# Kernel optimization log

Hardware: AMD Instinct MI355X
Metric: run time of the kernel (lower is better)

The kernel has to match this reference:

```python
import jax, jax.numpy as jnp
import numpy as np

P, F_IN, HG, C, T, E, HOUT = 4096, 64, 64, 64, 32, 65536, 12
LEAKY_SLOPE = 0.2
LN_EPS = 1e-5


def setup_inputs() -> dict:
    key = jax.random.key(0)
    ks = jax.random.split(key, 14)
    g = lambda k, shape, scale: (jax.random.normal(k, shape, jnp.float32) * scale)
    return {
        "X": jax.random.normal(ks[0], (1, P, F_IN, T), jnp.float32),
        "edge_index": jax.random.randint(ks[1], (T, 2, E), 0, P, jnp.int32),
        # GATv2 params (single head)
        "Wl": g(ks[2], (F_IN, HG), 0.1),
        "Wr": g(ks[3], (F_IN, HG), 0.1),
        "att": g(ks[4], (HG,), 0.1),
        "gat_b": g(ks[5], (HG,), 0.02),
        # 1x1 time conv (HG -> C) and 1x1 residual conv (F_IN -> C)
        "W_time": g(ks[6], (C, HG), 0.1),
        "b_time": g(ks[7], (C,), 0.02),
        "W_res": g(ks[8], (C, F_IN), 0.1),
        "b_res": g(ks[9], (C,), 0.02),
        # LayerNorm over channel dim C
        "ln_g": jnp.ones((C,), jnp.float32),
        "ln_b": jnp.zeros((C,), jnp.float32),
        # final conv: Conv2d(in=T, out=HOUT, kernel=(1, C)) -> weight (HOUT, T, C)
        "W_final": g(ks[10], (HOUT, T, C), 0.05),
        "b_final": g(ks[11], (HOUT,), 0.02),
    }


def reference(X, edge_index, Wl, Wr, att, gat_b, W_time, b_time, W_res, b_res,
              ln_g, ln_b, W_final, b_final):
    Pn = X.shape[1]

    def gat_t(x, edges):
        # x: (P, F_IN), edges: (2, E) with edges[0]=src j, edges[1]=dst i
        src, dst = edges[0], edges[1]
        hl = x @ Wl                      # (P, HG) messages
        hr = x @ Wr                      # (P, HG) query side
        e = jax.nn.leaky_relu(hl[src] + hr[dst], LEAKY_SLOPE) @ att  # (E,)
        emax = jax.ops.segment_max(e, dst, num_segments=Pn)
        ex = jnp.exp(e - emax[dst])
        den = jax.ops.segment_sum(ex, dst, num_segments=Pn)
        alpha = ex / den[dst]            # softmax over in-edges of each dst
        return jax.ops.segment_sum(alpha[:, None] * hl[src], dst,
                                   num_segments=Pn) + gat_b  # (P, HG)

    xs = jnp.moveaxis(X[0], -1, 0)                     # (T, P, F_IN)
    X_hat = jax.nn.relu(jax.vmap(gat_t)(xs, edge_index))  # (T, P, HG)

    th = jnp.einsum('tph,ch->tpc', X_hat, W_time) + b_time  # time conv 1x1
    rs = jnp.einsum('tpf,cf->tpc', xs, W_res) + b_res       # residual conv 1x1
    y = jax.nn.relu(th + rs)                                 # (T, P, C)

    mu = jnp.mean(y, axis=-1, keepdims=True)
    var = jnp.var(y, axis=-1, keepdims=True)
    yn = (y - mu) * jax.lax.rsqrt(var + LN_EPS) * ln_g + ln_b  # (T, P, C)

    # final conv: in-channels = T, kernel (1, C) -> contract over t and c
    out = jnp.einsum('tpc,otc->po', yn, W_final) + b_final     # (P, HOUT)
    return out[None]                                           # (1, P, HOUT)
```

## Files before the change

kernel.cpp:

```cpp
#include <hip/hip_runtime.h>
#include <math.h>

#define NP 4096
#define F_IN 64
#define HG 64
#define NC 64
#define NT 32
#define NE 65536
#define HOUT 12
#define LEAKY 0.2f
#define LN_EPS 1e-5f
#define CAPC 32

template <int CTRL>
__device__ __forceinline__ float dppadd(float v, float x) {
    int r = __builtin_amdgcn_update_dpp(0, __builtin_bit_cast(int, x), CTRL, 0xF, 0xF, false);
    return v + __builtin_bit_cast(float, r);
}
__device__ __forceinline__ float rowsum16(float v) {
    v = dppadd<0x128>(v, v);
    v = dppadd<0x124>(v, v);
    v = dppadd<0x122>(v, v);
    v = dppadd<0x121>(v, v);
    return v;
}
__device__ __forceinline__ float laneXorSum(float v) {
    v += __shfl_xor(v, 16, 64);
    v += __shfl_xor(v, 32, 64);
    return v;
}

#define FMA4(Acomp, B, r)                                                     \
    acc[r][0] += (Acomp) * (B).x; acc[r][1] += (Acomp) * (B).y;               \
    acc[r][2] += (Acomp) * (B).z; acc[r][3] += (Acomp) * (B).w;

__global__ __launch_bounds__(256) void k_front(const float* __restrict__ X,
        const float* __restrict__ Wl, const float* __restrict__ Wr,
        const float* __restrict__ W_res, const float* __restrict__ b_res,
        const float* __restrict__ W_time,
        const int* __restrict__ EI,
        float* __restrict__ hl, float* __restrict__ hr, float* __restrict__ rs,
        float* __restrict__ wtT,
        int* __restrict__ cnt, unsigned short* __restrict__ scap) {
    __shared__ float smem[9472];
    int b = blockIdx.x;
    int tid = threadIdx.x;
    if (b < 512) {
        unsigned short (*buck)[CAPC] = (unsigned short (*)[CAPC])smem;
        int* cnts = (int*)(smem + 8192);
        int t = (b & 7) + 8 * ((b >> 3) & 3);
        int rem = b >> 5;
        int c = rem & 1, r = rem >> 1;
        cnts[tid] = 0; cnts[tid + 256] = 0;
        __syncthreads();
        const int4* srcA = (const int4*)(EI + (size_t)t * 2 * NE) + c * (NE / 8);
        const int4* dstA = (const int4*)(EI + (size_t)t * 2 * NE + NE) + c * (NE / 8);
        for (int i = tid; i < NE / 8; i += 256) {
            int4 s = srcA[i];
            int4 d = dstA[i];
            if ((d.x >> 9) == r) { int lo = d.x & 511; int sl = atomicAdd(&cnts[lo], 1); if (sl < CAPC) buck[lo][sl] = (unsigned short)s.x; }
            if ((d.y >> 9) == r) { int lo = d.y & 511; int sl = atomicAdd(&cnts[lo], 1); if (sl < CAPC) buck[lo][sl] = (unsigned short)s.y; }
            if ((d.z >> 9) == r) { int lo = d.z & 511; int sl = atomicAdd(&cnts[lo], 1); if (sl < CAPC) buck[lo][sl] = (unsigned short)s.z; }
            if ((d.w >> 9) == r) { int lo = d.w & 511; int sl = atomicAdd(&cnts[lo], 1); if (sl < CAPC) buck[lo][sl] = (unsigned short)s.w; }
        }
        __syncthreads();
        int obase = ((t * 2 + c) << 12) + (r << 9);
        cnt[obase + tid] = cnts[tid];
        cnt[obase + tid + 256] = cnts[tid + 256];
        unsigned int* dstw = (unsigned int*)(scap + (size_t)obase * CAPC);
        const unsigned int* srcw = (const unsigned int*)buck;
        for (int i = tid; i < 512 * CAPC / 2; i += 256)
            dstw[i] = srcw[i];
    } else if (b < 2560) {
        float (*xs)[F_IN][40] = (float (*)[F_IN][40])smem;
        float (*bk)[68] = (float (*)[68])(smem + 5120);
        int p0 = (b - 512) * 2;
        const float4* Xp = (const float4*)(X + (size_t)p0 * F_IN * NT);
        for (int i4 = tid; i4 < 1024; i4 += 256) {
            int pp = i4 >> 9, f = (i4 >> 3) & 63, t0 = (i4 & 7) * 4;
            *(float4*)&xs[pp][f][t0] = Xp[i4];
        }
        int ng = tid & 15, pp = (tid >> 4) & 1, tg = tid >> 5;
        int n0 = ng * 4, t0 = tg * 4;
        {
            const float4* B4 = (const float4*)Wl;
            for (int i4 = tid; i4 < 1024; i4 += 256)
                *(float4*)&bk[i4 >> 4][(i4 & 15) * 4] = B4[i4];
            __syncthreads();
            float acc[4][4];
#pragma unroll
            for (int i = 0; i < 4; ++i)
#pragma unroll
                for (int j2 = 0; j2 < 4; ++j2) acc[i][j2] = 0.f;
#pragma unroll 8
            for (int f = 0; f < F_IN; ++f) {
                float4 B = *(const float4*)&bk[f][n0];
                float4 A = *(const float4*)&xs[pp][f][t0];
                FMA4(A.x, B, 0) FMA4(A.y, B, 1) FMA4(A.z, B, 2) FMA4(A.w, B, 3)
            }
#pragma unroll
            for (int i = 0; i < 4; ++i) {
                float4 v;
                v.x = acc[i][0]; v.y = acc[i][1]; v.z = acc[i][2]; v.w = acc[i][3];
                *(float4*)&hl[((size_t)(t0 + i) * NP + p0 + pp) * HG + n0] = v;
            }
            __syncthreads();
        }
        {
            const float4* B4 = (const float4*)Wr;
            for (int i4 = tid; i4 < 1024; i4 += 256)
                *(float4*)&bk[i4 >> 4][(i4 & 15) * 4] = B4[i4];
            __syncthreads();
            float acc[4][4];
#pragma unroll
            for (int i = 0; i < 4; ++i)
#pragma unroll
                for (int j2 = 0; j2 < 4; ++j2) acc[i][j2] = 0.f;
#pragma unroll 8
            for (int f = 0; f < F_IN; ++f) {
                float4 B = *(const float4*)&bk[f][n0];
                float4 A = *(const float4*)&xs[pp][f][t0];
                FMA4(A.x, B, 0) FMA4(A.y, B, 1) FMA4(A.z, B, 2) FMA4(A.w, B, 3)
            }
#pragma unroll
            for (int i = 0; i < 4; ++i) {
                float4 v;
                v.x = acc[i][0]; v.y = acc[i][1]; v.z = acc[i][2]; v.w = acc[i][3];
                *(float4*)&hr[((size_t)(t0 + i) * NP + p0 + pp) * HG + n0] = v;
            }
            __syncthreads();
        }
        {
            for (int i = tid; i < F_IN * NC; i += 256) {
                int c = i >> 6, f = i & 63;
                bk[f][c] = W_res[i];
            }
            __syncthreads();
            float4 br4 = *(const float4*)&b_res[n0];
            float acc[4][4];
#pragma unroll
            for (int i = 0; i < 4; ++i) {
                acc[i][0] = br4.x; acc[i][1] = br4.y; acc[i][2] = br4.z; acc[i][3] = br4.w;
            }
#pragma unroll 8
            for (int f = 0; f < F_IN; ++f) {
                float4 B = *(const float4*)&bk[f][n0];
                float4 A = *(const float4*)&xs[pp][f][t0];
                FMA4(A.x, B, 0) FMA4(A.y, B, 1) FMA4(A.z, B, 2) FMA4(A.w, B, 3)
            }
#pragma unroll
            for (int i = 0; i < 4; ++i) {
                float4 v;
                v.x = acc[i][0]; v.y = acc[i][1]; v.z = acc[i][2]; v.w = acc[i][3];
                *(float4*)&rs[((size_t)(t0 + i) * NP + p0 + pp) * NC + n0] = v;
            }
        }
    } else {
        int i = (b - 2560) * 256 + tid;
        wtT[i] = W_time[(i & 63) * 64 + (i >> 6)];
    }
}

__global__ __launch_bounds__(256) void k_gat(const float* __restrict__ hl,
        const float* __restrict__ hr, const float* __restrict__ rs,
        const int* __restrict__ cnt, const unsigned short* __restrict__ scap,
        const float* __restrict__ att, const float* __restrict__ gat_b,
        const float* __restrict__ wtT, const float* __restrict__ b_time,
        const float* __restrict__ ln_g, const float* __restrict__ ln_b,
        const float* __restrict__ Wf, float* __restrict__ pout) {
    __shared__ int sidx[4][8][64];
    __shared__ float xbuf[4][8][64];
    __shared__ int sdeg[4][8];
    __shared__ float wt[64][68];
    int b = blockIdx.x;
    int t = (b & 7) + 8 * (b >> 10);
    int pc = (b >> 3) & 127;
    int tid = threadIdx.x;
    int ws = tid >> 6;
    int lane = tid & 63;
    int row = lane >> 4;
    int cg = lane & 15;
    int c0 = cg * 4;
    const float4* w4s = (const float4*)wtT;
    for (int i4 = tid; i4 < 1024; i4 += 256)
        *(float4*)&wt[i4 >> 4][(i4 & 15) * 4] = w4s[i4];
    __syncthreads();
    float4 at4 = *(const float4*)&att[c0];
    float4 gb4 = *(const float4*)&gat_b[c0];
    float4 bt4 = *(const float4*)&b_time[c0];
    float4 lg  = *(const float4*)&ln_g[c0];
    float4 lb  = *(const float4*)&ln_b[c0];
    float4 wf0 = *(const float4*)&Wf[((size_t)(3 * row + 0) * NT + t) * NC + c0];
    float4 wf1 = *(const float4*)&Wf[((size_t)(3 * row + 1) * NT + t) * NC + c0];
    float4 wf2 = *(const float4*)&Wf[((size_t)(3 * row + 2) * NT + t) * NC + c0];
    int p0 = pc * 32 + ws * 8;
    const int* cb0 = cnt + ((t * 2 + 0) << 12) + p0;
    const int* cb1 = cnt + ((t * 2 + 1) << 12) + p0;
    const unsigned short* sb0 = scap + ((size_t)(((t * 2 + 0) << 12) + p0)) * CAPC;
    const unsigned short* sb1 = scap + ((size_t)(((t * 2 + 1) << 12) + p0)) * CAPC;
#pragma unroll
    for (int q = 0; q < 8; ++q) {
        int d0 = cb0[q]; d0 = (d0 < CAPC) ? d0 : CAPC;
        int d1 = cb1[q]; d1 = (d1 < CAPC) ? d1 : CAPC;
        int deg = d0 + d1;
        if (lane == 0) sdeg[ws][q] = deg;
        int li = (lane < deg) ? lane : 0;
        int f1 = (li >= d0);
        int idx = f1 ? (li - d0) : li;
        const unsigned short* sp = f1 ? (sb1 + q * CAPC) : (sb0 + q * CAPC);
        sidx[ws][q][lane] = (int)sp[idx];
    }
    const float* hlt = hl + (size_t)t * NP * HG;
    for (int q = 0; q < 8; ++q) {
        int p = p0 + q;
        float4 r4 = *(const float4*)&hr[((size_t)t * NP + p) * HG + c0];
        int deg = sdeg[ws][q];
        float l = 0.f;
        float4 acc = {0.f, 0.f, 0.f, 0.f};
        int nfull = deg & ~7;
        int j = 0;
        for (; j < nfull; j += 8) {
            int src0 = sidx[ws][q][j + row];
            int src1 = sidx[ws][q][j + 4 + row];
            float4 h0 = *(const float4*)&hlt[((size_t)src0 << 6) + c0];
            float4 h1 = *(const float4*)&hlt[((size_t)src1 << 6) + c0];
            float4 z0, z1;
            z0.x = h0.x + r4.x; z0.y = h0.y + r4.y; z0.z = h0.z + r4.z; z0.w = h0.w + r4.w;
            z1.x = h1.x + r4.x; z1.y = h1.y + r4.y; z1.z = h1.z + r4.z; z1.w = h1.w + r4.w;
            z0.x = fmaxf(z0.x, LEAKY * z0.x); z0.y = fmaxf(z0.y, LEAKY * z0.y);
            z0.z = fmaxf(z0.z, LEAKY * z0.z); z0.w = fmaxf(z0.w, LEAKY * z0.w);
            z1.x = fmaxf(z1.x, LEAKY * z1.x); z1.y = fmaxf(z1.y, LEAKY * z1.y);
            z1.z = fmaxf(z1.z, LEAKY * z1.z); z1.w = fmaxf(z1.w, LEAKY * z1.w);
            float e0 = rowsum16(z0.x * at4.x + z0.y * at4.y + z0.z * at4.z + z0.w * at4.w);
            float e1 = rowsum16(z1.x * at4.x + z1.y * at4.y + z1.z * at4.z + z1.w * at4.w);
            float w0 = __expf(e0);
            float w1 = __expf(e1);
            l += w0 + w1;
            acc.x += w0 * h0.x + w1 * h1.x;
            acc.y += w0 * h0.y + w1 * h1.y;
            acc.z += w0 * h0.z + w1 * h1.z;
            acc.w += w0 * h0.w + w1 * h1.w;
        }
        for (; j < deg; j += 4) {
            int jj = j + row;
            int src = sidx[ws][q][(jj < deg) ? jj : 0];
            float4 ha = *(const float4*)&hlt[((size_t)src << 6) + c0];
            float4 za;
            za.x = ha.x + r4.x; za.y = ha.y + r4.y; za.z = ha.z + r4.z; za.w = ha.w + r4.w;
            za.x = fmaxf(za.x, LEAKY * za.x);
            za.y = fmaxf(za.y, LEAKY * za.y);
            za.z = fmaxf(za.z, LEAKY * za.z);
            za.w = fmaxf(za.w, LEAKY * za.w);
            float ep = za.x * at4.x + za.y * at4.y + za.z * at4.z + za.w * at4.w;
            float e = rowsum16(ep);
            float w = __expf(e);
            w = (jj < deg) ? w : 0.f;
            l += w;
            acc.x += w * ha.x; acc.y += w * ha.y; acc.z += w * ha.z; acc.w += w * ha.w;
        }
        float lt = laneXorSum(l);
        acc.x = laneXorSum(acc.x);
        acc.y = laneXorSum(acc.y);
        acc.z = laneXorSum(acc.z);
        acc.w = laneXorSum(acc.w);
        float inv = (deg > 0) ? (1.0f / lt) : 0.f;
        float4 xh;
        xh.x = fmaxf(acc.x * inv + gb4.x, 0.f);
        xh.y = fmaxf(acc.y * inv + gb4.y, 0.f);
        xh.z = fmaxf(acc.z * inv + gb4.z, 0.f);
        xh.w = fmaxf(acc.w * inv + gb4.w, 0.f);
        if (row == 0) *(float4*)&xbuf[ws][q][c0] = xh;
    }
    float4 y[8];
#pragma unroll
    for (int q = 0; q < 8; ++q) { y[q].x = 0.f; y[q].y = 0.f; y[q].z = 0.f; y[q].w = 0.f; }
#pragma unroll
    for (int i4 = 0; i4 < 4; ++i4) {
        int h0 = row * 16 + i4 * 4;
        float4 w0 = *(const float4*)&wt[h0 + 0][c0];
        float4 w1 = *(const float4*)&wt[h0 + 1][c0];
        float4 w2 = *(const float4*)&wt[h0 + 2][c0];
        float4 w3 = *(const float4*)&wt[h0 + 3][c0];
#pragma unroll
        for (int q = 0; q < 8; ++q) {
            float4 xf = *(const float4*)&xbuf[ws][q][h0];
            y[q].x += xf.x * w0.x + xf.y * w1.x + xf.z * w2.x + xf.w * w3.x;
            y[q].y += xf.x * w0.y + xf.y * w1.y + xf.z * w2.y + xf.w * w3.y;
            y[q].z += xf.x * w0.z + xf.y * w1.z + xf.z * w2.z + xf.w * w3.z;
            y[q].w += xf.x * w0.w + xf.y * w1.w + xf.z * w2.w + xf.w * w3.w;
        }
    }
#pragma unroll
    for (int q = 0; q < 8; ++q) {
        float ya = laneXorSum(y[q].x);
        float yb = laneXorSum(y[q].y);
        float yc = laneXorSum(y[q].z);
        float yd = laneXorSum(y[q].w);
        float4 rs4 = *(const float4*)&rs[((size_t)t * NP + p0 + q) * NC + c0];
        float y0 = fmaxf(ya + bt4.x + rs4.x, 0.f);
        float y1 = fmaxf(yb + bt4.y + rs4.y, 0.f);
        float y2 = fmaxf(yc + bt4.z + rs4.z, 0.f);
        float y3 = fmaxf(yd + bt4.w + rs4.w, 0.f);
        float s  = rowsum16(y0 + y1 + y2 + y3);
        float ss = rowsum16(y0 * y0 + y1 * y1 + y2 * y2 + y3 * y3);
        float mu = s * (1.f / 64.f);
        float var = ss * (1.f / 64.f) - mu * mu;
        float rsd = rsqrtf(var + LN_EPS);
        float n0 = (y0 - mu) * rsd * lg.x + lb.x;
        float n1 = (y1 - mu) * rsd * lg.y + lb.y;
        float n2 = (y2 - mu) * rsd * lg.z + lb.z;
        float n3 = (y3 - mu) * rsd * lg.w + lb.w;
        float o0 = n0 * wf0.x + n1 * wf0.y + n2 * wf0.z + n3 * wf0.w;
        float o1 = n0 * wf1.x + n1 * wf1.y + n2 * wf1.z + n3 * wf1.w;
        float o2 = n0 * wf2.x + n1 * wf2.y + n2 * wf2.z + n3 * wf2.w;
        o0 = rowsum16(o0); o1 = rowsum16(o1); o2 = rowsum16(o2);
        if (cg == 0) {
            xbuf[ws][q][3 * row + 0] = o0;
            xbuf[ws][q][3 * row + 1] = o1;
            xbuf[ws][q][3 * row + 2] = o2;
        }
    }
    float* pb = pout + ((size_t)t * NP + p0) * HOUT;
    for (int k = lane; k < 96; k += 64)
        pb[k] = xbuf[ws][k / 12][k % 12];
}

__global__ __launch_bounds__(256) void k_out(const float* __restrict__ pout,
        const float* __restrict__ bf, float* __restrict__ out) {
    int k = blockIdx.x * 256 + threadIdx.x;
    float s = bf[k % HOUT];
#pragma unroll 8
    for (int t = 0; t < NT; ++t) s += pout[(size_t)t * (NP * HOUT) + k];
    out[k] = s;
}

extern "C" void kernel_launch(void* const* d_in, const int* in_sizes, int n_in,
                              void* d_out, int out_size, void* d_ws, size_t ws_size,
                              hipStream_t stream) {
    const float* X      = (const float*)d_in[0];
    const int*   EI     = (const int*)d_in[1];
    const float* Wl     = (const float*)d_in[2];
    const float* Wr     = (const float*)d_in[3];
    const float* att    = (const float*)d_in[4];
    const float* gat_b  = (const float*)d_in[5];
    const float* W_time = (const float*)d_in[6];
    const float* b_time = (const float*)d_in[7];
    const float* W_res  = (const float*)d_in[8];
    const float* b_res  = (const float*)d_in[9];
    const float* ln_g   = (const float*)d_in[10];
    const float* ln_b   = (const float*)d_in[11];
    const float* Wf     = (const float*)d_in[12];
    const float* bf     = (const float*)d_in[13];
    float* out = (float*)d_out;

    char* ws = (char*)d_ws;
    const size_t MB = 1024 * 1024;
    float* hl   = (float*)(ws);
    float* hr   = (float*)(ws + 32 * MB);
    float* rs   = (float*)(ws + 64 * MB);
    float* wtT  = (float*)(ws + 96 * MB);
    int*   cnt  = (int*)  (ws + 97 * MB);
    unsigned short* scap = (unsigned short*)(ws + 98 * MB);
    float* pout = (float*)(ws + 114 * MB);

    k_front<<<2576, 256, 0, stream>>>(X, Wl, Wr, W_res, b_res, W_time, EI,
                                      hl, hr, rs, wtT, cnt, scap);
    k_gat  <<<4096, 256, 0, stream>>>(hl, hr, rs, cnt, scap, att, gat_b,
                                      wtT, b_time, ln_g, ln_b, Wf, pout);
    k_out  <<<NP * HOUT / 256, 256, 0, stream>>>(pout, bf, out);
}
```

Measured before the change: 323.5 us.

## Stream per-node GAT epilogue, fold LayerNorm into final conv, raise occupancy

The k_gat kernel now runs the time-conv, LayerNorm and final-conv epilogue for each destination node right after its attention aggregation, instead of batching eight nodes in registers and shared memory. LayerNorm gain and bias are folded algebraically into the final-conv weights (per-row sums S and B), so normalized values are never materialized. Shared memory shrinks and launch bounds request 8 blocks per CU to raise occupancy and hide gather latency. The risks are register spills under the tighter register budget and a redundant duplicated setup block.

Result: slower. 754.5 us (+133.2%).

```diff
diff --git a/kernel.cpp b/kernel.cpp
--- a/kernel.cpp
+++ b/kernel.cpp
@@ -161,17 +161,17 @@
     }
 }
 
-__global__ __launch_bounds__(256) void k_gat(const float* __restrict__ hl,
+__global__ __launch_bounds__(256, 8) void k_gat(const float* __restrict__ hl,
         const float* __restrict__ hr, const float* __restrict__ rs,
         const int* __restrict__ cnt, const unsigned short* __restrict__ scap,
         const float* __restrict__ att, const float* __restrict__ gat_b,
         const float* __restrict__ wtT, const float* __restrict__ b_time,
         const float* __restrict__ ln_g, const float* __restrict__ ln_b,
         const float* __restrict__ Wf, float* __restrict__ pout) {
-    __shared__ int sidx[4][8][64];
-    __shared__ float xbuf[4][8][64];
-    __shared__ int sdeg[4][8];
-    __shared__ float wt[64][68];
+    __shared__ float wt[64][64];
+    __shared__ int   sidx[4][64];
+    __shared__ float xbuf[4][64];
+    __shared__ float obuf[4][96];
     int b = blockIdx.x;
     int t = (b & 7) + 8 * (b >> 10);
     int pc = (b >> 3) & 127;
@@ -188,40 +188,61 @@
     float4 at4 = *(const float4*)&att[c0];
     float4 gb4 = *(const float4*)&gat_b[c0];
     float4 bt4 = *(const float4*)&b_time[c0];
-    float4 lg  = *(const float4*)&ln_g[c0];
-    float4 lb  = *(const float4*)&ln_b[c0];
-    float4 wf0 = *(const float4*)&Wf[((size_t)(3 * row + 0) * NT + t) * NC + c0];
-    float4 wf1 = *(const float4*)&Wf[((size_t)(3 * row + 1) * NT + t) * NC + c0];
-    float4 wf2 = *(const float4*)&Wf[((size_t)(3 * row + 2) * NT + t) * NC + c0];
+    float4 G0, G1, G2;
+    float S0, S1, S2, B0, B1, B2;
+    {
+        float4 lg = *(const float4*)&ln_g[c0];
+        float4 lb = *(const float4*)&ln_b[c0];
+        float4 wfa = *(const float4*)&Wf[((size_t)(3 * row + 0) * NT + t) * NC + c0];
+        float4 wfb = *(const float4*)&Wf[((size_t)(3 * row + 1) * NT + t) * NC + c0];
+        float4 wfc = *(const float4*)&Wf[((size_t)(3 * row + 2) * NT + t) * NC + c0];
+        G0.x = lg.x * wfa.x; G0.y = lg.y * wfa.y; G0.z = lg.z * wfa.z; G0.w = lg.w * wfa.w;
+        G1.x = lg.x * wfb.x; G1.y = lg.y * wfb.y; G1.z = lg.z * wfb.z; G1.w = lg.w * wfb.w;
+        G2.x = lg.x * wfc.x; G2.y = lg.y * wfc.y; G2.z = lg.z * wfc.z; G2.w = lg.w * wfc.w;
+        S0 = __builtin_amdgcn_readfirstlane(__shfl(rowsum16(G0.x + G0.y + G0.z + G0.w), row * 16, 64));
+        S1 = __builtin_amdgcn_readfirstlane(__shfl(rowsum16(G1.x + G1.y + G1.z + G1.w), row * 16, 64));
+        S2 = __builtin_amdgcn_readfirstlane(__shfl(rowsum16(G2.x + G2.y + G2.z + G2.w), row * 16, 64));
+        B0 = __builtin_amdgcn_readfirstlane(__shfl(rowsum16(lb.x * wfa.x + lb.y * wfa.y + lb.z * wfa.z + lb.w * wfa.w), row * 16, 64));
+        B1 = __builtin_amdgcn_readfirstlane(__shfl(rowsum16(lb.x * wfb.x + lb.y * wfb.y + lb.z * wfb.z + lb.w * wfb.w), row * 16, 64));
+        B2 = __builtin_amdgcn_readfirstlane(__shfl(rowsum16(lb.x * wfc.x + lb.y * wfc.y + lb.z * wfc.z + lb.w * wfc.w), row * 16, 64));
+    }
+    {
+        float4 lg = *(const float4*)&ln_g[c0];
+        float4 lb = *(const float4*)&ln_b[c0];
+        float4 wfa = *(const float4*)&Wf[((size_t)(3 * row + 0) * NT + t) * NC + c0];
+        float4 wfb = *(const float4*)&Wf[((size_t)(3 * row + 1) * NT + t) * NC + c0];
+        float4 wfc = *(const float4*)&Wf[((size_t)(3 * row + 2) * NT + t) * NC + c0];
+        S0 = rowsum16(G0.x + G0.y + G0.z + G0.w);
+        S1 = rowsum16(G1.x + G1.y + G1.z + G1.w);
+        S2 = rowsum16(G2.x + G2.y + G2.z + G2.w);
+        B0 = rowsum16(lb.x * wfa.x + lb.y * wfa.y + lb.z * wfa.z + lb.w * wfa.w);
+        B1 = rowsum16(lb.x * wfb.x + lb.y * wfb.y + lb.z * wfb.z + lb.w * wfb.w);
+        B2 = rowsum16(lb.x * wfc.x + lb.y * wfc.y + lb.z * wfc.z + lb.w * wfc.w);
+    }
     int p0 = pc * 32 + ws * 8;
     const int* cb0 = cnt + ((t * 2 + 0) << 12) + p0;
     const int* cb1 = cnt + ((t * 2 + 1) << 12) + p0;
     const unsigned short* sb0 = scap + ((size_t)(((t * 2 + 0) << 12) + p0)) * CAPC;
     const unsigned short* sb1 = scap + ((size_t)(((t * 2 + 1) << 12) + p0)) * CAPC;
-#pragma unroll
+    const float* hlt = hl + (size_t)t * NP * HG;
     for (int q = 0; q < 8; ++q) {
+        int p = p0 + q;
         int d0 = cb0[q]; d0 = (d0 < CAPC) ? d0 : CAPC;
         int d1 = cb1[q]; d1 = (d1 < CAPC) ? d1 : CAPC;
         int deg = d0 + d1;
-        if (lane == 0) sdeg[ws][q] = deg;
         int li = (lane < deg) ? lane : 0;
         int f1 = (li >= d0);
         int idx = f1 ? (li - d0) : li;
         const unsigned short* sp = f1 ? (sb1 + q * CAPC) : (sb0 + q * CAPC);
-        sidx[ws][q][lane] = (int)sp[idx];
-    }
-    const float* hlt = hl + (size_t)t * NP * HG;
-    for (int q = 0; q < 8; ++q) {
-        int p = p0 + q;
+        sidx[ws][lane] = (int)sp[idx];
         float4 r4 = *(const float4*)&hr[((size_t)t * NP + p) * HG + c0];
-        int deg = sdeg[ws][q];
         float l = 0.f;
         float4 acc = {0.f, 0.f, 0.f, 0.f};
         int nfull = deg & ~7;
         int j = 0;
         for (; j < nfull; j += 8) {
-            int src0 = sidx[ws][q][j + row];
-            int src1 = sidx[ws][q][j + 4 + row];
+            int src0 = sidx[ws][j + row];
+            int src1 = sidx[ws][j + 4 + row];
             float4 h0 = *(const float4*)&hlt[((size_t)src0 << 6) + c0];
             float4 h1 = *(const float4*)&hlt[((size_t)src1 << 6) + c0];
             float4 z0, z1;
@@ -243,7 +264,7 @@
         }
         for (; j < deg; j += 4) {
             int jj = j + row;
-            int src = sidx[ws][q][(jj < deg) ? jj : 0];
+            int src = sidx[ws][(jj < deg) ? jj : 0];
             float4 ha = *(const float4*)&hlt[((size_t)src << 6) + c0];
             float4 za;
             za.x = ha.x + r4.x; za.y = ha.y + r4.y; za.z = ha.z + r4.z; za.w = ha.w + r4.w;
@@ -269,34 +290,20 @@
         xh.y = fmaxf(acc.y * inv + gb4.y, 0.f);
         xh.z = fmaxf(acc.z * inv + gb4.z, 0.f);
         xh.w = fmaxf(acc.w * inv + gb4.w, 0.f);
-        if (row == 0) *(float4*)&xbuf[ws][q][c0] = xh;
-    }
-    float4 y[8];
-#pragma unroll
-    for (int q = 0; q < 8; ++q) { y[q].x = 0.f; y[q].y = 0.f; y[q].z = 0.f; y[q].w = 0.f; }
-#pragma unroll
-    for (int i4 = 0; i4 < 4; ++i4) {
-        int h0 = row * 16 + i4 * 4;
-        float4 w0 = *(const float4*)&wt[h0 + 0][c0];
-        float4 w1 = *(const float4*)&wt[h0 + 1][c0];
-        float4 w2 = *(const float4*)&wt[h0 + 2][c0];
-        float4 w3 = *(const float4*)&wt[h0 + 3][c0];
-#pragma unroll
-        for (int q = 0; q < 8; ++q) {
-            float4 xf = *(const float4*)&xbuf[ws][q][h0];
-            y[q].x += xf.x * w0.x + xf.y * w1.x + xf.z * w2.x + xf.w * w3.x;
-            y[q].y += xf.x * w0.y + xf.y * w1.y + xf.z * w2.y + xf.w * w3.y;
-            y[q].z += xf.x * w0.z + xf.y * w1.z + xf.z * w2.z + xf.w * w3.z;
-            y[q].w += xf.x * w0.w + xf.y * w1.w + xf.z * w2.w + xf.w * w3.w;
-        }
-    }
-#pragma unroll
-    for (int q = 0; q < 8; ++q) {
-        float ya = laneXorSum(y[q].x);
-        float yb = laneXorSum(y[q].y);
-        float yc = laneXorSum(y[q].z);
-        float yd = laneXorSum(y[q].w);
-        float4 rs4 = *(const float4*)&rs[((size_t)t * NP + p0 + q) * NC + c0];
+        if (row == 0) *(float4*)&xbuf[ws][c0] = xh;
+        float4 y4 = {0.f, 0.f, 0.f, 0.f};
+#pragma unroll
+        for (int i = 0; i < 16; ++i) {
+            int h = row * 16 + i;
+            float xf = xbuf[ws][h];
+            float4 w = *(const float4*)&wt[h][c0];
+            y4.x += xf * w.x; y4.y += xf * w.y; y4.z += xf * w.z; y4.w += xf * w.w;
+        }
+        float ya = laneXorSum(y4.x);
+        float yb = laneXorSum(y4.y);
+        float yc = laneXorSum(y4.z);
+        float yd = laneXorSum(y4.w);
+        float4 rs4 = *(const float4*)&rs[((size_t)t * NP + p) * NC + c0];
         float y0 = fmaxf(ya + bt4.x + rs4.x, 0.f);
         float y1 = fmaxf(yb + bt4.y + rs4.y, 0.f);
         float y2 = fmaxf(yc + bt4.z + rs4.z, 0.f);
@@ -306,23 +313,21 @@
         float mu = s * (1.f / 64.f);
         float var = ss * (1.f / 64.f) - mu * mu;
         float rsd = rsqrtf(var + LN_EPS);
-        float n0 = (y0 - mu) * rsd * lg.x + lb.x;
-        float n1 = (y1 - mu) * rsd * lg.y + lb.y;
-        float n2 = (y2 - mu) * rsd * lg.z + lb.z;
-        float n3 = (y3 - mu) * rsd * lg.w + lb.w;
-        float o0 = n0 * wf0.x + n1 * wf0.y + n2 * wf0.z + n3 * wf0.w;
-        float o1 = n0 * wf1.x + n1 * wf1.y + n2 * wf1.z + n3 * wf1.w;
-        float o2 = n0 * wf2.x + n1 * wf2.y + n2 * wf2.z + n3 * wf2.w;
-        o0 = rowsum16(o0); o1 = rowsum16(o1); o2 = rowsum16(o2);
+        float U0 = rowsum16(y0 * G0.x + y1 * G0.y + y2 * G0.z + y3 * G0.w);
+        float U1 = rowsum16(y0 * G1.x + y1 * G1.y + y2 * G1.z + y3 * G1.w);
+        float U2 = rowsum16(y0 * G2.x + y1 * G2.y + y2 * G2.z + y3 * G2.w);
+        float o0 = (U0 - mu * S0) * rsd + B0;
+        float o1 = (U1 - mu * S1) * rsd + B1;
+        float o2 = (U2 - mu * S2) * rsd + B2;
         if (cg == 0) {
-            xbuf[ws][q][3 * row + 0] = o0;
-            xbuf[ws][q][3 * row + 1] = o1;
-            xbuf[ws][q][3 * row + 2] = o2;
+            obuf[ws][q * 12 + 3 * row + 0] = o0;
+            obuf[ws][q * 12 + 3 * row + 1] = o1;
+            obuf[ws][q * 12 + 3 * row + 2] = o2;
         }
     }
     float* pb = pout + ((size_t)t * NP + p0) * HOUT;
-    for (int k = lane; k < 96; k += 64)
-        pb[k] = xbuf[ws][k / 12][k % 12];
+    pb[lane] = obuf[ws][lane];
+    if (lane < 32) pb[64 + lane] = obuf[ws][64 + lane];
 }
 
 __global__ __launch_bounds__(256) void k_out(const float* __restrict__ pout,
```
